# Kernel tuning notes

Hardware: AMD Instinct MI355X
Metric: run time of the kernel (lower is better)

## Reference

```python
import jax, jax.numpy as jnp
import numpy as np

H, DH = 16, 64          # num_heads, dim_head
DIM = 1024              # dim_ltn
EPS = 1e-5


def setup_inputs() -> dict:
    key = jax.random.key(0)
    ks = jax.random.split(key, 8)
    b, n_txt, t, m = 2, 2048, 4, 256
    text = jax.random.normal(ks[0], (b, n_txt, DIM), dtype=jnp.float32)
    image = jax.random.normal(ks[1], (b, t, m, DIM), dtype=jnp.float32)
    locations = jax.random.randint(ks[2], (b, n_txt), 0, 2)  # 0/1 media markers
    s = DIM ** -0.5
    Wq = jax.random.normal(ks[3], (DIM, H * DH), dtype=jnp.float32) * s
    Wkv = jax.random.normal(ks[4], (DIM, 2 * H * DH), dtype=jnp.float32) * s
    Wo = jax.random.normal(ks[5], (H * DH, DIM), dtype=jnp.float32) * s
    ln_gamma = jnp.ones((DIM,), dtype=jnp.float32)
    ln_beta = jnp.zeros((DIM,), dtype=jnp.float32)
    return {"text": text, "image": image, "locations": locations,
            "Wq": Wq, "Wkv": Wkv, "Wo": Wo,
            "ln_gamma": ln_gamma, "ln_beta": ln_beta}


def reference(text, image, locations, Wq, Wkv, Wo, ln_gamma, ln_beta):
    scale = DH ** -0.5
    b, t, m, d = image.shape
    # LayerNorm(text)
    mu = text.mean(-1, keepdims=True)
    var = ((text - mu) ** 2).mean(-1, keepdims=True)
    tn = (text - mu) / jnp.sqrt(var + EPS) * ln_gamma + ln_beta
    img = image.reshape(b, t * m, d)             # b (t m) d
    q = tn @ Wq                                  # b n (h dh)
    k, v = jnp.split(img @ Wkv, 2, axis=-1)      # each b tm (h dh)
    split_heads = lambda x: x.reshape(x.shape[0], x.shape[1], H, DH).transpose(0, 2, 1, 3)
    q, k, v = split_heads(q), split_heads(k), split_heads(v)
    attn = jnp.einsum('bhid,bhjd->bhij', q, k) * scale   # b h n (t m)
    txt_time = jnp.cumsum(locations, axis=-1)            # b n : media index per text token
    viz_time = jnp.repeat(jnp.arange(1, t + 1), m)       # (t m)
    # only_attend_to_immediate -> equality mask
    mask = txt_time[:, None, :, None] == viz_time[None, None, None, :]
    neg = -jnp.finfo(attn.dtype).max
    attn = jnp.where(mask, attn, neg)
    attn = jax.nn.softmax(attn, axis=-1)
    # zero attention for text tokens before any media (txt_time == 0)
    attn = jnp.where((txt_time == 0)[:, None, :, None], 0.0, attn)
    out = jnp.einsum('bhij,bhjd->bhid', attn, v)
    out = out.transpose(0, 2, 1, 3).reshape(b, -1, H * DH)
    return out @ Wo
```

## Files before the change

kernel.cpp:

```cpp
#include <hip/hip_runtime.h>

#define BATCH 2
#define NTXT  2048
#define TMED  4
#define MMED  256
#define TM    (TMED * MMED)
#define DIM   1024
#define NH    16
#define DHD   64
#define KVW   2048
#define RMAX  256
#define QSTR  ((size_t)BATCH * RMAX * DIM)

typedef _Float16 f16x8 __attribute__((ext_vector_type(8)));
typedef float    f32x4 __attribute__((ext_vector_type(4)));

__global__ __launch_bounds__(256) void k1_prep(
    const int* __restrict__ loc, const float* __restrict__ Wkv,
    int* __restrict__ tt, int* __restrict__ seg, float* __restrict__ vbar,
    _Float16* __restrict__ WkvT) {
  __shared__ float tile[64][65];
  __shared__ int tots[256];
  __shared__ int s_start, s_end;
  const int bid = blockIdx.x;
  const int tid = threadIdx.x;
  if (bid < BATCH) {
    const int b = bid;
    if (tid == 0) { s_start = NTXT; s_end = NTXT; }
    __syncthreads();
    int v[8];
    int run = 0;
    const int base = b * NTXT + tid * 8;
#pragma unroll
    for (int k = 0; k < 8; k++) { run += loc[base + k]; v[k] = run; }
    tots[tid] = run; __syncthreads();
    for (int off = 1; off < 256; off <<= 1) {
      const int add = (tid >= off) ? tots[tid - off] : 0;
      __syncthreads();
      tots[tid] += add;
      __syncthreads();
    }
    const int excl = tots[tid] - run;
#pragma unroll
    for (int k = 0; k < 8; k++) {
      const int tv = excl + v[k];
      tt[base + k] = tv;
      if (tv >= 1) atomicMin(&s_start, tid * 8 + k);
      if (tv >= 5) atomicMin(&s_end, tid * 8 + k);
    }
    __syncthreads();
    if (tid == 0) {
      seg[b * 2]     = s_start;
      seg[b * 2 + 1] = s_end - s_start;
    }
  } else if (bid == 2) {
    for (int c = tid; c < 2 * BATCH * DIM; c += 256) vbar[c] = 0.f;
  } else {
    const int idx = bid - 3;
    const int k0 = (idx & 15) * 64, n0 = (idx >> 4) * 64;
    const int r = tid >> 4, c4 = (tid & 15) * 4;
#pragma unroll
    for (int i = 0; i < 4; i++) {
      const float4 v = *reinterpret_cast<const float4*>(
          Wkv + (size_t)(k0 + r + i * 16) * KVW + n0 + c4);
      tile[r + i * 16][c4 + 0] = v.x; tile[r + i * 16][c4 + 1] = v.y;
      tile[r + i * 16][c4 + 2] = v.z; tile[r + i * 16][c4 + 3] = v.w;
    }
    __syncthreads();
#pragma unroll
    for (int it = 0; it < 2; it++) {
      const int chunk = it * 256 + tid;
      const int n = chunk >> 3, kc = (chunk & 7) * 8;
      f16x8 h;
#pragma unroll
      for (int j = 0; j < 8; j++) h[j] = (_Float16)tile[kc + j][n];
      *reinterpret_cast<f16x8*>(WkvT + (size_t)(n0 + n) * DIM + k0 + kc) = h;
    }
  }
}

__global__ __launch_bounds__(512) void k2_gemm_qproj(
    const float* __restrict__ image, const _Float16* __restrict__ WkvT,
    const float* __restrict__ text, const float* __restrict__ Wq,
    const float* __restrict__ gamma, const float* __restrict__ beta,
    const int* __restrict__ seg, _Float16* __restrict__ kv16,
    float* __restrict__ qpart, float* __restrict__ vbar) {
  __shared__ char smem[16384];
  const int idx = blockIdx.x;
  const int tid = threadIdx.x;
  if (idx < 256) {
    _Float16* As = (_Float16*)smem;
    _Float16* Bs = As + 128 * 32;
    const int lane = tid & 63, wid = tid >> 6;
    const int wm = wid & 3, wn = wid >> 2;
    const int row0 = (idx >> 4) * 128, col0 = (idx & 15) * 128;
    const int srow = tid >> 2, skc = (tid & 3) * 8;
    const int frow = lane & 15, fq = lane >> 4;
    f32x4 acc[2][4] = {};
    for (int k0 = 0; k0 < DIM; k0 += 32) {
      const float* ap = image + (size_t)(row0 + srow) * DIM + k0 + skc;
      const float4 a0 = *reinterpret_cast<const float4*>(ap);
      const float4 a1 = *reinterpret_cast<const float4*>(ap + 4);
      f16x8 av;
      av[0] = (_Float16)a0.x; av[1] = (_Float16)a0.y;
      av[2] = (_Float16)a0.z; av[3] = (_Float16)a0.w;
      av[4] = (_Float16)a1.x; av[5] = (_Float16)a1.y;
      av[6] = (_Float16)a1.z; av[7] = (_Float16)a1.w;
      const f16x8 bv = *reinterpret_cast<const f16x8*>(
          WkvT + (size_t)(col0 + srow) * DIM + k0 + skc);
      __syncthreads();
      *reinterpret_cast<f16x8*>(As + tid * 8) = av;
      *reinterpret_cast<f16x8*>(Bs + tid * 8) = bv;
      __syncthreads();
      f16x8 af[2], bf[4];
#pragma unroll
      for (int mt = 0; mt < 2; mt++)
        af[mt] = *reinterpret_cast<const f16x8*>(
            As + (wm * 32 + mt * 16 + frow) * 32 + fq * 8);
#pragma unroll
      for (int nt = 0; nt < 4; nt++)
        bf[nt] = *reinterpret_cast<const f16x8*>(
            Bs + (wn * 64 + nt * 16 + frow) * 32 + fq * 8);
#pragma unroll
      for (int mt = 0; mt < 2; mt++)
#pragma unroll
        for (int nt = 0; nt < 4; nt++)
          acc[mt][nt] = __builtin_amdgcn_mfma_f32_16x16x32_f16(
              af[mt], bf[nt], acc[mt][nt], 0, 0, 0);
    }
#pragma unroll
    for (int mt = 0; mt < 2; mt++)
#pragma unroll
      for (int nt = 0; nt < 4; nt++) {
        const int col = col0 + wn * 64 + nt * 16 + frow;
#pragma unroll
        for (int r = 0; r < 4; r++) {
          const int row = row0 + wm * 32 + mt * 16 + fq * 4 + r;
          kv16[(size_t)row * KVW + col] = (_Float16)acc[mt][nt][r];
        }
      }
    if (col0 >= DIM) {
      const int b = row0 >> 10;
#pragma unroll
      for (int nt = 0; nt < 4; nt++) {
        float s = 0.f;
#pragma unroll
        for (int mt = 0; mt < 2; mt++)
#pragma unroll
          for (int r = 0; r < 4; r++) s += acc[mt][nt][r];
        s += __shfl_down(s, 32);
        s += __shfl_down(s, 16);
        if (lane < 16)
          atomicAdd(&vbar[b * DIM + (col0 - DIM) + wn * 64 + nt * 16 + lane],
                    s * (1.0f / (float)TM));
      }
    }
  } else {
    float* tn_s = (float*)smem;
    const int j = idx - 256;
    const int b = j >> 5, nt = (j >> 2) & 7, cc = j & 3;
    const int n0 = nt * 128, c0 = cc * 256;
    const int lane = tid & 63, w = tid >> 6;
    const int n = tid & 127, rp = tid >> 7;
    const int i0 = seg[b * 2];
    const int cnt = min(seg[b * 2 + 1], RMAX);
    float* qp = qpart + (size_t)cc * QSTR;
    for (int r0 = 0; r0 < cnt; r0 += 8) {
      const int rows = min(8, cnt - r0);
      if (w < rows) {
        const float* xrow = text + (size_t)(b * NTXT + i0 + r0 + w) * DIM;
        float s = 0.f, sq = 0.f;
#pragma unroll
        for (int u = 0; u < 16; u++) {
          const float x = xrow[lane + 64 * u];
          s += x; sq += x * x;
        }
#pragma unroll
        for (int off = 32; off > 0; off >>= 1) {
          s += __shfl_xor(s, off);
          sq += __shfl_xor(sq, off);
        }
        const float mu = s * (1.0f / DIM);
        const float rstd = rsqrtf(sq * (1.0f / DIM) - mu * mu + 1e-5f);
#pragma unroll
        for (int u = 0; u < 4; u++) {
          const int c = c0 + lane + 64 * u;
          tn_s[w * 256 + lane + 64 * u] =
              (xrow[c] - mu) * rstd * gamma[c] + beta[c];
        }
      }
      __syncthreads();
      float a0 = 0.f, a1 = 0.f;
      for (int c = 0; c < 256; c++) {
        const float wv = Wq[(size_t)(c0 + c) * DIM + n0 + n];
        a0 += tn_s[(rp * 2) * 256 + c] * wv;
        a1 += tn_s[(rp * 2 + 1) * 256 + c] * wv;
      }
      if (rp * 2 < rows)
        qp[(size_t)(b * RMAX + r0 + rp * 2) * DIM + n0 + n] = a0;
      if (rp * 2 + 1 < rows)
        qp[(size_t)(b * RMAX + r0 + rp * 2 + 1) * DIM + n0 + n] = a1;
      __syncthreads();
    }
  }
}

__global__ __launch_bounds__(512) void k3_obar_zero(
    const float* __restrict__ vbar, const float* __restrict__ Wo,
    const int* __restrict__ seg, float* __restrict__ obar,
    float* __restrict__ out) {
  __shared__ float vb_s[128];
  const int bid = blockIdx.x;
  const int tid = threadIdx.x;
  if (bid < 32) {
    const int b = bid >> 4, et = (bid >> 3) & 1, cc = bid & 7;
    const int e = et * 512 + tid, c0 = cc * 128;
    if (tid < 128) vb_s[tid] = vbar[b * DIM + c0 + tid];
    __syncthreads();
    float s = 0.f;
    for (int c = 0; c < 128; c++)
      s += vb_s[c] * Wo[(size_t)(c0 + c) * DIM + e];
    atomicAdd(&obar[b * DIM + e], s);
  } else {
    const int b = bid - 32;
    const int i0 = seg[b * 2];
    const int cnt = min(seg[b * 2 + 1], RMAX);
    for (int r = 0; r < cnt; r++) {
      float* orow = out + (size_t)(b * NTXT + i0 + r) * DIM;
      orow[tid] = 0.f;
      orow[tid + 512] = 0.f;
    }
  }
}

__global__ __launch_bounds__(256) void k4_fill_attn(
    const float* __restrict__ text, const _Float16* __restrict__ kv16,
    const float* __restrict__ Wq, const float* __restrict__ Wo,
    const float* __restrict__ gamma, const float* __restrict__ beta,
    const int* __restrict__ tt, const int* __restrict__ seg,
    const float* __restrict__ obar, const float* __restrict__ qpart,
    float* __restrict__ out) {
  __shared__ float red[256];
  __shared__ float pbuf[256];
  const int idx = blockIdx.x;
  const int tid = threadIdx.x;
  if (idx < BATCH * NTXT) {
    const int b = idx >> 11;
    const int i = idx & (NTXT - 1);
    const int t = tt[idx];
    float* orow = out + (size_t)idx * DIM;
    if (t == 0) {
      *reinterpret_cast<float4*>(&orow[tid * 4]) =
          make_float4(0.f, 0.f, 0.f, 0.f);
      return;
    }
    if (t > TMED) {
      *reinterpret_cast<float4*>(&orow[tid * 4]) =
          *reinterpret_cast<const float4*>(&obar[b * DIM + tid * 4]);
      return;
    }
    if (i - seg[b * 2] < RMAX) return;
    __shared__ float tns[DIM];
    __shared__ float qrow[DIM];
    __shared__ float oaccs[DIM];
    const float* xrow = text + (size_t)idx * DIM;
    float x[4];
    float s = 0.f;
#pragma unroll
    for (int u = 0; u < 4; u++) { x[u] = xrow[tid + 256 * u]; s += x[u]; }
    red[tid] = s; __syncthreads();
    for (int st = 128; st > 0; st >>= 1) {
      if (tid < st) red[tid] += red[tid + st];
      __syncthreads();
    }
    const float mu = red[0] * (1.0f / DIM); __syncthreads();
    float vs = 0.f;
#pragma unroll
    for (int u = 0; u < 4; u++) { float d = x[u] - mu; vs += d * d; }
    red[tid] = vs; __syncthreads();
    for (int st = 128; st > 0; st >>= 1) {
      if (tid < st) red[tid] += red[tid + st];
      __syncthreads();
    }
    const float rstd = rsqrtf(red[0] * (1.0f / DIM) + 1e-5f); __syncthreads();
#pragma unroll
    for (int u = 0; u < 4; u++) {
      const int c = tid + 256 * u;
      tns[c] = (x[u] - mu) * rstd * gamma[c] + beta[c];
    }
    __syncthreads();
    {
      float qa[4] = {0.f, 0.f, 0.f, 0.f};
      for (int c = 0; c < DIM; c++) {
        const float tv = tns[c];
        const float* wp = Wq + (size_t)c * DIM + tid;
#pragma unroll
        for (int u = 0; u < 4; u++) qa[u] += tv * wp[256 * u];
      }
#pragma unroll
      for (int u = 0; u < 4; u++) qrow[tid + 256 * u] = qa[u];
    }
    __syncthreads();
    const size_t kvrow0 = (size_t)(b * TM + (t - 1) * MMED) * KVW;
    const int d0 = tid & 63, g = tid >> 6;
    for (int h = 0; h < NH; h++) {
      const _Float16* krow = kv16 + kvrow0 + (size_t)tid * KVW + h * DHD;
      float sc = 0.f;
#pragma unroll
      for (int d = 0; d < DHD; d++) sc += qrow[h * DHD + d] * (float)krow[d];
      sc *= 0.125f;
      red[tid] = sc; __syncthreads();
      for (int st = 128; st > 0; st >>= 1) {
        if (tid < st) red[tid] = fmaxf(red[tid], red[tid + st]);
        __syncthreads();
      }
      const float mx = red[0]; __syncthreads();
      const float e = __expf(sc - mx);
      red[tid] = e; __syncthreads();
      for (int st = 128; st > 0; st >>= 1) {
        if (tid < st) red[tid] += red[tid + st];
        __syncthreads();
      }
      const float inv = 1.0f / red[0]; __syncthreads();
      pbuf[tid] = e * inv; __syncthreads();
      const _Float16* vbase =
          kv16 + kvrow0 + (size_t)(g * 64) * KVW + DIM + h * DHD + d0;
      float a = 0.f;
#pragma unroll 8
      for (int jj = 0; jj < 64; jj++)
        a += pbuf[g * 64 + jj] * (float)vbase[(size_t)jj * KVW];
      red[tid] = a; __syncthreads();
      if (tid < 64)
        oaccs[h * DHD + tid] =
            red[tid] + red[64 + tid] + red[128 + tid] + red[192 + tid];
      __syncthreads();
    }
    float oa[4] = {0.f, 0.f, 0.f, 0.f};
    for (int c = 0; c < DIM; c++) {
      const float ov = oaccs[c];
      const float* wp = Wo + (size_t)c * DIM + tid;
#pragma unroll
      for (int u = 0; u < 4; u++) oa[u] += ov * wp[256 * u];
    }
#pragma unroll
    for (int u = 0; u < 4; u++) orow[tid + 256 * u] = oa[u];
  } else {
    __shared__ float qs[DHD];
    __shared__ float oacc_s[DHD];
    const int j = idx - BATCH * NTXT;
    const int h = j & 15, rt = (j >> 4) & 31, b = j >> 9;
    const int i0 = seg[b * 2];
    const int cnt = min(seg[b * 2 + 1], RMAX);
    const int d0 = tid & 63, g = tid >> 6;
    for (int r = rt; r < cnt; r += 32) {
      const int i = i0 + r;
      const int t = tt[b * NTXT + i];
      if (tid < 64) {
        const size_t qoff = (size_t)(b * RMAX + r) * DIM + h * DHD + tid;
        qs[tid] = qpart[qoff] + qpart[QSTR + qoff] +
                  qpart[2 * QSTR + qoff] + qpart[3 * QSTR + qoff];
      }
      __syncthreads();
      const size_t kvrow0 = (size_t)(b * TM + (t - 1) * MMED) * KVW;
      const _Float16* krow = kv16 + kvrow0 + (size_t)tid * KVW + h * DHD;
      float sc = 0.f;
#pragma unroll
      for (int d = 0; d < DHD; d += 8) {
        const f16x8 kk = *reinterpret_cast<const f16x8*>(krow + d);
#pragma unroll
        for (int u = 0; u < 8; u++) sc += qs[d + u] * (float)kk[u];
      }
      sc *= 0.125f;
      red[tid] = sc; __syncthreads();
      for (int st = 128; st > 0; st >>= 1) {
        if (tid < st) red[tid] = fmaxf(red[tid], red[tid + st]);
        __syncthreads();
      }
      const float mx = red[0]; __syncthreads();
      const float e = __expf(sc - mx);
      red[tid] = e; __syncthreads();
      for (int st = 128; st > 0; st >>= 1) {
        if (tid < st) red[tid] += red[tid + st];
        __syncthreads();
      }
      const float inv = 1.0f / red[0]; __syncthreads();
      pbuf[tid] = e * inv; __syncthreads();
      const _Float16* vbase =
          kv16 + kvrow0 + (size_t)(g * 64) * KVW + DIM + h * DHD + d0;
      float a = 0.f;
#pragma unroll 8
      for (int jj = 0; jj < 64; jj++)
        a += pbuf[g * 64 + jj] * (float)vbase[(size_t)jj * KVW];
      red[tid] = a; __syncthreads();
      if (tid < 64)
        oacc_s[tid] = red[tid] + red[64 + tid] + red[128 + tid] + red[192 + tid];
      __syncthreads();
      float* orow = out + (size_t)(b * NTXT + i) * DIM;
#pragma unroll
      for (int u = 0; u < 4; u++) {
        const int e2 = tid + 256 * u;
        float s2 = 0.f;
#pragma unroll 8
        for (int d = 0; d < DHD; d++)
          s2 += oacc_s[d] * Wo[(size_t)(h * DHD + d) * DIM + e2];
        atomicAdd(&orow[e2], s2);
      }
      __syncthreads();
    }
  }
}

extern "C" void kernel_launch(void* const* d_in, const int* in_sizes, int n_in,
                              void* d_out, int out_size, void* d_ws, size_t ws_size,
                              hipStream_t stream) {
  const float* text  = (const float*)d_in[0];
  const float* image = (const float*)d_in[1];
  const int*   loc   = (const int*)d_in[2];
  const float* Wq    = (const float*)d_in[3];
  const float* Wkv   = (const float*)d_in[4];
  const float* Wo    = (const float*)d_in[5];
  const float* gamma = (const float*)d_in[6];
  const float* beta  = (const float*)d_in[7];
  float* out = (float*)d_out;

  _Float16* kv16  = (_Float16*)d_ws;
  _Float16* WkvT  = kv16 + (size_t)BATCH * TM * KVW;
  float*    qpart = (float*)(WkvT + (size_t)KVW * DIM);
  float*    vbar  = qpart + 4 * QSTR;
  float*    obar  = vbar + BATCH * DIM;
  int*      tt    = (int*)(obar + BATCH * DIM);
  int*      seg   = tt + BATCH * NTXT;

  k1_prep<<<515, 256, 0, stream>>>(loc, Wkv, tt, seg, vbar, WkvT);
  k2_gemm_qproj<<<320, 512, 0, stream>>>(image, WkvT, text, Wq, gamma, beta,
                                         seg, kv16, qpart, vbar);
  k3_obar_zero<<<34, 512, 0, stream>>>(vbar, Wo, seg, obar, out);
  k4_fill_attn<<<BATCH * NTXT + NH * 32 * BATCH, 256, 0, stream>>>(
      text, kv16, Wq, Wo, gamma, beta, tt, seg, obar, qpart, out);
}
```

Measured before the change: 182.4 us.

## Shrink KV GEMM tiles, stage attention output, add separate O-projection kernel

The KV projection GEMM drops from 128x128 tiles with 512 threads to 64x64 tiles with 256 threads, giving many more blocks. The q-projection blocks move to the front of the grid and process 4 rows per pass. The attention tail no longer does a per-head Wo projection with atomicAdd into out. It writes the per-row head outputs to a workspace that reuses the WkvT region, and a new k5 kernel computes the output projection with plain stores, so the zeroing pass in k3 goes away. This is meant to remove atomic traffic and improve load balance, at the cost of an extra launch and an intermediate buffer round trip.

After: 187.2 us. 1.03x slower.

```diff
diff --git a/kernel.cpp b/kernel.cpp
--- a/kernel.cpp
+++ b/kernel.cpp
@@ -79,24 +79,25 @@
   }
 }
 
-__global__ __launch_bounds__(512) void k2_gemm_qproj(
+__global__ __launch_bounds__(256) void k2_gemm_qproj(
     const float* __restrict__ image, const _Float16* __restrict__ WkvT,
     const float* __restrict__ text, const float* __restrict__ Wq,
     const float* __restrict__ gamma, const float* __restrict__ beta,
     const int* __restrict__ seg, _Float16* __restrict__ kv16,
     float* __restrict__ qpart, float* __restrict__ vbar) {
-  __shared__ char smem[16384];
+  __shared__ char smem[8192];
   const int idx = blockIdx.x;
   const int tid = threadIdx.x;
-  if (idx < 256) {
+  if (idx >= 64) {
     _Float16* As = (_Float16*)smem;
-    _Float16* Bs = As + 128 * 32;
+    _Float16* Bs = As + 64 * 32;
+    const int gid = idx - 64;
     const int lane = tid & 63, wid = tid >> 6;
-    const int wm = wid & 3, wn = wid >> 2;
-    const int row0 = (idx >> 4) * 128, col0 = (idx & 15) * 128;
+    const int wm = wid & 1, wn = wid >> 1;
+    const int row0 = (gid >> 5) * 64, col0 = (gid & 31) * 64;
     const int srow = tid >> 2, skc = (tid & 3) * 8;
     const int frow = lane & 15, fq = lane >> 4;
-    f32x4 acc[2][4] = {};
+    f32x4 acc[2][2] = {};
     for (int k0 = 0; k0 < DIM; k0 += 32) {
       const float* ap = image + (size_t)(row0 + srow) * DIM + k0 + skc;
       const float4 a0 = *reinterpret_cast<const float4*>(ap);
@@ -112,27 +113,27 @@
       *reinterpret_cast<f16x8*>(As + tid * 8) = av;
       *reinterpret_cast<f16x8*>(Bs + tid * 8) = bv;
       __syncthreads();
-      f16x8 af[2], bf[4];
+      f16x8 af[2], bf[2];
 #pragma unroll
       for (int mt = 0; mt < 2; mt++)
         af[mt] = *reinterpret_cast<const f16x8*>(
             As + (wm * 32 + mt * 16 + frow) * 32 + fq * 8);
 #pragma unroll
-      for (int nt = 0; nt < 4; nt++)
+      for (int nt = 0; nt < 2; nt++)
         bf[nt] = *reinterpret_cast<const f16x8*>(
-            Bs + (wn * 64 + nt * 16 + frow) * 32 + fq * 8);
+            Bs + (wn * 32 + nt * 16 + frow) * 32 + fq * 8);
 #pragma unroll
       for (int mt = 0; mt < 2; mt++)
 #pragma unroll
-        for (int nt = 0; nt < 4; nt++)
+        for (int nt = 0; nt < 2; nt++)
           acc[mt][nt] = __builtin_amdgcn_mfma_f32_16x16x32_f16(
               af[mt], bf[nt], acc[mt][nt], 0, 0, 0);
     }
 #pragma unroll
     for (int mt = 0; mt < 2; mt++)
 #pragma unroll
-      for (int nt = 0; nt < 4; nt++) {
-        const int col = col0 + wn * 64 + nt * 16 + frow;
+      for (int nt = 0; nt < 2; nt++) {
+        const int col = col0 + wn * 32 + nt * 16 + frow;
 #pragma unroll
         for (int r = 0; r < 4; r++) {
           const int row = row0 + wm * 32 + mt * 16 + fq * 4 + r;
@@ -142,7 +143,7 @@
     if (col0 >= DIM) {
       const int b = row0 >> 10;
 #pragma unroll
-      for (int nt = 0; nt < 4; nt++) {
+      for (int nt = 0; nt < 2; nt++) {
         float s = 0.f;
 #pragma unroll
         for (int mt = 0; mt < 2; mt++)
@@ -151,22 +152,22 @@
         s += __shfl_down(s, 32);
         s += __shfl_down(s, 16);
         if (lane < 16)
-          atomicAdd(&vbar[b * DIM + (col0 - DIM) + wn * 64 + nt * 16 + lane],
+          atomicAdd(&vbar[b * DIM + (col0 - DIM) + wn * 32 + nt * 16 + lane],
                     s * (1.0f / (float)TM));
       }
     }
   } else {
     float* tn_s = (float*)smem;
-    const int j = idx - 256;
+    const int j = idx;
     const int b = j >> 5, nt = (j >> 2) & 7, cc = j & 3;
     const int n0 = nt * 128, c0 = cc * 256;
     const int lane = tid & 63, w = tid >> 6;
-    const int n = tid & 127, rp = tid >> 7;
+    const int n = tid & 127, rh = tid >> 7;
     const int i0 = seg[b * 2];
     const int cnt = min(seg[b * 2 + 1], RMAX);
     float* qp = qpart + (size_t)cc * QSTR;
-    for (int r0 = 0; r0 < cnt; r0 += 8) {
-      const int rows = min(8, cnt - r0);
+    for (int r0 = 0; r0 < cnt; r0 += 4) {
+      const int rows = min(4, cnt - r0);
       if (w < rows) {
         const float* xrow = text + (size_t)(b * NTXT + i0 + r0 + w) * DIM;
         float s = 0.f, sq = 0.f;
@@ -193,44 +194,32 @@
       float a0 = 0.f, a1 = 0.f;
       for (int c = 0; c < 256; c++) {
         const float wv = Wq[(size_t)(c0 + c) * DIM + n0 + n];
-        a0 += tn_s[(rp * 2) * 256 + c] * wv;
-        a1 += tn_s[(rp * 2 + 1) * 256 + c] * wv;
-      }
-      if (rp * 2 < rows)
-        qp[(size_t)(b * RMAX + r0 + rp * 2) * DIM + n0 + n] = a0;
-      if (rp * 2 + 1 < rows)
-        qp[(size_t)(b * RMAX + r0 + rp * 2 + 1) * DIM + n0 + n] = a1;
+        a0 += tn_s[(rh * 2) * 256 + c] * wv;
+        a1 += tn_s[(rh * 2 + 1) * 256 + c] * wv;
+      }
+      if (rh * 2 < rows)
+        qp[(size_t)(b * RMAX + r0 + rh * 2) * DIM + n0 + n] = a0;
+      if (rh * 2 + 1 < rows)
+        qp[(size_t)(b * RMAX + r0 + rh * 2 + 1) * DIM + n0 + n] = a1;
       __syncthreads();
     }
   }
 }
 
-__global__ __launch_bounds__(512) void k3_obar_zero(
+__global__ __launch_bounds__(512) void k3_obar(
     const float* __restrict__ vbar, const float* __restrict__ Wo,
-    const int* __restrict__ seg, float* __restrict__ obar,
-    float* __restrict__ out) {
+    float* __restrict__ obar) {
   __shared__ float vb_s[128];
   const int bid = blockIdx.x;
   const int tid = threadIdx.x;
-  if (bid < 32) {
-    const int b = bid >> 4, et = (bid >> 3) & 1, cc = bid & 7;
-    const int e = et * 512 + tid, c0 = cc * 128;
-    if (tid < 128) vb_s[tid] = vbar[b * DIM + c0 + tid];
-    __syncthreads();
-    float s = 0.f;
-    for (int c = 0; c < 128; c++)
-      s += vb_s[c] * Wo[(size_t)(c0 + c) * DIM + e];
-    atomicAdd(&obar[b * DIM + e], s);
-  } else {
-    const int b = bid - 32;
-    const int i0 = seg[b * 2];
-    const int cnt = min(seg[b * 2 + 1], RMAX);
-    for (int r = 0; r < cnt; r++) {
-      float* orow = out + (size_t)(b * NTXT + i0 + r) * DIM;
-      orow[tid] = 0.f;
-      orow[tid + 512] = 0.f;
-    }
-  }
+  const int b = bid >> 4, et = (bid >> 3) & 1, cc = bid & 7;
+  const int e = et * 512 + tid, c0 = cc * 128;
+  if (tid < 128) vb_s[tid] = vbar[b * DIM + c0 + tid];
+  __syncthreads();
+  float s = 0.f;
+  for (int c = 0; c < 128; c++)
+    s += vb_s[c] * Wo[(size_t)(c0 + c) * DIM + e];
+  atomicAdd(&obar[b * DIM + e], s);
 }
 
 __global__ __launch_bounds__(256) void k4_fill_attn(
@@ -239,7 +228,7 @@
     const float* __restrict__ gamma, const float* __restrict__ beta,
     const int* __restrict__ tt, const int* __restrict__ seg,
     const float* __restrict__ obar, const float* __restrict__ qpart,
-    float* __restrict__ out) {
+    float* __restrict__ oacc, float* __restrict__ out) {
   __shared__ float red[256];
   __shared__ float pbuf[256];
   const int idx = blockIdx.x;
@@ -346,7 +335,6 @@
     for (int u = 0; u < 4; u++) orow[tid + 256 * u] = oa[u];
   } else {
     __shared__ float qs[DHD];
-    __shared__ float oacc_s[DHD];
     const int j = idx - BATCH * NTXT;
     const int h = j & 15, rt = (j >> 4) & 31, b = j >> 9;
     const int i0 = seg[b * 2];
@@ -393,20 +381,34 @@
         a += pbuf[g * 64 + jj] * (float)vbase[(size_t)jj * KVW];
       red[tid] = a; __syncthreads();
       if (tid < 64)
-        oacc_s[tid] = red[tid] + red[64 + tid] + red[128 + tid] + red[192 + tid];
-      __syncthreads();
-      float* orow = out + (size_t)(b * NTXT + i) * DIM;
-#pragma unroll
-      for (int u = 0; u < 4; u++) {
-        const int e2 = tid + 256 * u;
-        float s2 = 0.f;
-#pragma unroll 8
-        for (int d = 0; d < DHD; d++)
-          s2 += oacc_s[d] * Wo[(size_t)(h * DHD + d) * DIM + e2];
-        atomicAdd(&orow[e2], s2);
-      }
-      __syncthreads();
-    }
+        oacc[(size_t)(b * RMAX + r) * DIM + h * DHD + tid] =
+            red[tid] + red[64 + tid] + red[128 + tid] + red[192 + tid];
+      __syncthreads();
+    }
+  }
+}
+
+__global__ __launch_bounds__(256) void k5_oproj(
+    const float* __restrict__ oacc, const float* __restrict__ Wo,
+    const int* __restrict__ seg, float* __restrict__ out) {
+  const int ct = blockIdx.x;
+  const int rt = blockIdx.y;
+  const int b = blockIdx.z;
+  const int i0 = seg[b * 2];
+  const int cnt = min(seg[b * 2 + 1], RMAX);
+  const int tid = threadIdx.x;
+  const int d0 = tid & 63, g = tid >> 6;
+  __shared__ float op[4][64];
+  for (int r = rt; r < cnt; r += 32) {
+    const float* arow = oacc + (size_t)(b * RMAX + r) * DIM;
+    const float* wo = Wo + (size_t)(g * 256) * DIM + ct * 64 + d0;
+    float s = 0.f;
+    for (int c = 0; c < 256; c++) s += arow[g * 256 + c] * wo[(size_t)c * DIM];
+    op[g][d0] = s; __syncthreads();
+    if (tid < 64)
+      out[(size_t)(b * NTXT + i0 + r) * DIM + ct * 64 + tid] =
+          op[0][tid] + op[1][tid] + op[2][tid] + op[3][tid];
+    __syncthreads();
   }
 }
 
@@ -425,6 +427,7 @@
 
   _Float16* kv16  = (_Float16*)d_ws;
   _Float16* WkvT  = kv16 + (size_t)BATCH * TM * KVW;
+  float*    oacc  = (float*)WkvT;
   float*    qpart = (float*)(WkvT + (size_t)KVW * DIM);
   float*    vbar  = qpart + 4 * QSTR;
   float*    obar  = vbar + BATCH * DIM;
@@ -432,9 +435,10 @@
   int*      seg   = tt + BATCH * NTXT;
 
   k1_prep<<<515, 256, 0, stream>>>(loc, Wkv, tt, seg, vbar, WkvT);
-  k2_gemm_qproj<<<320, 512, 0, stream>>>(image, WkvT, text, Wq, gamma, beta,
-                                         seg, kv16, qpart, vbar);
-  k3_obar_zero<<<34, 512, 0, stream>>>(vbar, Wo, seg, obar, out);
+  k2_gemm_qproj<<<1088, 256, 0, stream>>>(image, WkvT, text, Wq, gamma, beta,
+                                          seg, kv16, qpart, vbar);
+  k3_obar<<<32, 512, 0, stream>>>(vbar, Wo, obar);
   k4_fill_attn<<<BATCH * NTXT + NH * 32 * BATCH, 256, 0, stream>>>(
-      text, kv16, Wq, Wo, gamma, beta, tt, seg, obar, qpart, out);
-}
+      text, kv16, Wq, Wo, gamma, beta, tt, seg, obar, qpart, oacc, out);
+  k5_oproj<<<dim3(16, 32, BATCH), 256, 0, stream>>>(oacc, Wo, seg, out);
+}
```
